# Performance work log

Hardware: AMD Instinct MI355X
Metric: run time of the kernel (lower is better)

Reference implementation:

```python
import jax, jax.numpy as jnp
import numpy as np

B, TE, TD, HE, HD = 16, 512, 64, 512, 512


def setup_inputs() -> dict:
    key = jax.random.key(0)
    k1, k2, k3, k4, k5 = jax.random.split(key, 5)
    return {
        "encoder_out_seq": jax.random.normal(k1, (B, TE, HE), dtype=jnp.float32),
        "decoder_out_seq": jax.random.normal(k2, (B, TD, HD), dtype=jnp.float32),
        "W_a": jax.random.normal(k3, (HE, HE), dtype=jnp.float32) * 0.05,
        "U_a": jax.random.normal(k4, (HD, HE), dtype=jnp.float32) * 0.05,
        "V_a": jax.random.normal(k5, (HE, 1), dtype=jnp.float32) * 0.05,
    }


def reference(encoder_out_seq, decoder_out_seq, W_a, U_a, V_a):
    # Bahdanau additive attention, batched over all decoder steps at once
    # (the original K.rnn loop over Td is embarrassingly parallel).
    Ws = jnp.einsum('bte,eh->bth', encoder_out_seq, W_a)   # [B,Te,He]
    Uh = jnp.einsum('bdk,kh->bdh', decoder_out_seq, U_a)   # [B,Td,He]
    # additive combine + tanh: [B,Td,Te,He]
    act = jnp.tanh(Ws[:, None, :, :] + Uh[:, :, None, :])
    e = jnp.einsum('bdth,h->bdt', act, V_a[:, 0])          # [B,Td,Te]
    e = jax.nn.softmax(e, axis=-1)                          # attention weights
    c = jnp.einsum('bdt,bth->bdh', e, encoder_out_seq)      # [B,Td,He] context
    return (c, e)
```

## Files before the change

kernel.cpp:

```cpp
#include <hip/hip_runtime.h>
#include <hip/hip_bf16.h>

#define BB 16
#define TE 512
#define TD 64
#define HE 512

#define PRESCALE 2.8853900817779268f

typedef __attribute__((ext_vector_type(8))) short bf16x8;
typedef __attribute__((ext_vector_type(4))) float f32x4;

__device__ __forceinline__ float fexp2(float x) {
#if __has_builtin(__builtin_amdgcn_exp2f)
    return __builtin_amdgcn_exp2f(x);
#else
    return exp2f(x);
#endif
}
__device__ __forceinline__ float frcp(float x) {
#if __has_builtin(__builtin_amdgcn_rcpf)
    return __builtin_amdgcn_rcpf(x);
#else
    return __fdividef(1.f, x);
#endif
}

__device__ __forceinline__ void split2(float x, unsigned short& h, unsigned short& l) {
    __hip_bfloat16 hb = __float2bfloat16(x);
    h = *(unsigned short*)&hb;
    float r = x - __bfloat162float(hb);
    __hip_bfloat16 lb = __float2bfloat16(r);
    l = *(unsigned short*)&lb;
}

__device__ __forceinline__ void gload16(const unsigned short* g, void* l) {
    __builtin_amdgcn_global_load_lds(
        (const __attribute__((address_space(1))) unsigned int*)g,
        (__attribute__((address_space(3))) unsigned int*)l, 16, 0, 0);
}



__device__ __forceinline__ void tile_load(const float* __restrict__ src, int ld,
                                          float (*tile)[64], int tid)
{
#pragma unroll
    for (int p = 0; p < 4; ++p) {
        const int f = p * 256 + tid;
        const int r = f >> 4, c4 = f & 15;
        const float4 v = *(const float4*)&src[(size_t)r * ld + c4 * 4];
        *(float4*)&tile[r][((c4 ^ (r & 7))) << 2] = v;
    }
}

__device__ __forceinline__ void tile_outA(float (*tile)[64],
                                          unsigned short* __restrict__ H,
                                          unsigned short* __restrict__ L,
                                          size_t Ms, size_t sg_base, size_t m_base, int tid)
{
#pragma unroll
    for (int p = 0; p < 2; ++p) {
        const int task = p * 256 + tid;
        const int s = task >> 6, mm = task & 63;
        const float4 x = *(const float4*)&tile[mm][(((s << 1)    ) ^ (mm & 7)) << 2];
        const float4 y = *(const float4*)&tile[mm][(((s << 1) | 1) ^ (mm & 7)) << 2];
        ushort4 ha, la, hb, lb;
        split2(x.x, ha.x, la.x); split2(x.y, ha.y, la.y);
        split2(x.z, ha.z, la.z); split2(x.w, ha.w, la.w);
        split2(y.x, hb.x, lb.x); split2(y.y, hb.y, lb.y);
        split2(y.z, hb.z, lb.z); split2(y.w, hb.w, lb.w);
        const size_t o = ((sg_base + s) * Ms + m_base + mm) * 8;
        *(ushort4*)&H[o] = ha; *(ushort4*)&H[o + 4] = hb;
        *(ushort4*)&L[o] = la; *(ushort4*)&L[o + 4] = lb;
    }
}

__device__ __forceinline__ void tile_outT(float (*tile)[64],
                                          unsigned short* __restrict__ H,
                                          unsigned short* __restrict__ L,
                                          size_t Ns, size_t sg_base, size_t n_base, int tid)
{
#pragma unroll
    for (int p = 0; p < 2; ++p) {
        const int task = p * 256 + tid;
        const int s2 = task >> 6, hh = task & 63;
        float v[8];
#pragma unroll
        for (int q = 0; q < 8; ++q) {
            const int r = s2 * 8 + q;
            v[q] = tile[r][((((hh >> 2)) ^ (r & 7)) << 2) + (hh & 3)];
        }
        ushort4 ha, la, hb, lb;
        split2(v[0], ha.x, la.x); split2(v[1], ha.y, la.y);
        split2(v[2], ha.z, la.z); split2(v[3], ha.w, la.w);
        split2(v[4], hb.x, lb.x); split2(v[5], hb.y, lb.y);
        split2(v[6], hb.z, lb.z); split2(v[7], hb.w, lb.w);
        const size_t o = ((sg_base + s2) * Ns + n_base + hh) * 8;
        *(ushort4*)&H[o] = ha; *(ushort4*)&H[o + 4] = hb;
        *(ushort4*)&L[o] = la; *(ushort4*)&L[o + 4] = lb;
    }
}

__global__ __launch_bounds__(256)
void split_enc_k8(const float* __restrict__ X,
                  unsigned short* __restrict__ Ah, unsigned short* __restrict__ Al,
                  unsigned short* __restrict__ Th, unsigned short* __restrict__ Tl)
{
    __shared__ float tile[64][64];
    const int tid = threadIdx.x;
    const int h0 = blockIdx.x * 64, t0 = blockIdx.y * 64, b = blockIdx.z;
    const size_t bo = (size_t)b * TE * HE;

    tile_load(X + bo + (size_t)t0 * HE + h0, HE, tile, tid);
    __syncthreads();

    tile_outA(tile, Ah, Al, (size_t)BB * TE, h0 >> 3, (size_t)b * TE + t0, tid);
    tile_outT(tile, Th + bo, Tl + bo, HE, t0 >> 3, h0, tid);
}

__global__ __launch_bounds__(256)
void split_misc_k8(const float* __restrict__ dec,
                   unsigned short* __restrict__ dH, unsigned short* __restrict__ dL,
                   const float* __restrict__ Wa,
                   unsigned short* __restrict__ wH, unsigned short* __restrict__ wL,
                   const float* __restrict__ Ua,
                   unsigned short* __restrict__ uH, unsigned short* __restrict__ uL)
{
    __shared__ float tile[64][64];
    const int tid = threadIdx.x;
    const int z = blockIdx.z;

    if (z == 2) {
        const int m0 = blockIdx.y * 64, h0 = blockIdx.x * 64;
        tile_load(dec + (size_t)m0 * HE + h0, HE, tile, tid);
        __syncthreads();
        tile_outA(tile, dH, dL, (size_t)BB * TD, h0 >> 3, m0, tid);
        return;
    }
    if (blockIdx.y >= 8) return;
    const float* X = z ? Ua : Wa;
    unsigned short* H = z ? uH : wH;
    unsigned short* L = z ? uL : wL;
    const int r0 = blockIdx.y * 64, c0 = blockIdx.x * 64;
    tile_load(X + (size_t)r0 * HE + c0, HE, tile, tid);
    __syncthreads();
    tile_outT(tile, H, L, HE, r0 >> 3, c0, tid);
}

__global__ __launch_bounds__(256)
void gemm_ws_uh(const unsigned short* __restrict__ eAh, const unsigned short* __restrict__ eAl,
                const unsigned short* __restrict__ wBh, const unsigned short* __restrict__ wBl,
                float* __restrict__ Ew,
                const unsigned short* __restrict__ dAh, const unsigned short* __restrict__ dAl,
                const unsigned short* __restrict__ uBh, const unsigned short* __restrict__ uBl,
                float* __restrict__ Eu)
{
    __shared__ char smem[2][32768];

    const int tid  = threadIdx.x;
    const int lane = tid & 63;
    const int wave = tid >> 6;
    const int wr = wave >> 1, wc = wave & 1;
    const int fr = lane & 15, fg = lane >> 4;

    const unsigned short *Ahi, *Alo, *Bhi, *Blo;
    float* C;
    int M, row0;
    if (blockIdx.y < 64) {
        Ahi = eAh; Alo = eAl; Bhi = wBh; Blo = wBl; C = Ew;
        M = BB * TE; row0 = blockIdx.y * 128;
    } else {
        Ahi = dAh; Alo = dAl; Bhi = uBh; Blo = uBl; C = Eu;
        M = BB * TD; row0 = (blockIdx.y - 64) * 128;
    }
    const int N = HE, K = HE;
    const int col0 = blockIdx.x * 128;

    f32x4 acc[4][4];
#pragma unroll
    for (int mi = 0; mi < 4; ++mi)
#pragma unroll
        for (int ni = 0; ni < 4; ++ni)
            acc[mi][ni] = (f32x4){0.f, 0.f, 0.f, 0.f};

    auto STAGE = [&](int buf, int k0) {
#pragma unroll
        for (int c = 0; c < 2; ++c) {
            const int bi  = (c * 4 + wave) * 64 + lane;
            const int g   = bi >> 7;
            const int idx = bi & 127;
            int mrow = row0 + idx; if (mrow >= M) mrow -= M;
            const int ncol = col0 + idx;
            const size_t ao = ((size_t)((k0 >> 3) + g) * M + mrow) * 8;
            const size_t bo = ((size_t)((k0 >> 3) + g) * N + ncol) * 8;
            const int lb = (c * 4 + wave) * 1024;
            gload16(Ahi + ao, smem[buf] + lb);
            gload16(Alo + ao, smem[buf] + 8192 + lb);
            gload16(Bhi + bo, smem[buf] + 16384 + lb);
            gload16(Blo + bo, smem[buf] + 24576 + lb);
        }
    };

    STAGE(0, 0);

    int buf = 0;
    for (int k0 = 0; k0 < K; k0 += 32) {
        if (k0 + 32 < K) {
            STAGE(buf ^ 1, k0 + 32);
            asm volatile("s_waitcnt vmcnt(8)\n\ts_barrier" ::: "memory");
        } else {
            asm volatile("s_waitcnt vmcnt(0)\n\ts_barrier" ::: "memory");
        }

        const int gb = fg << 7;
        bf16x8 ah[4], al[4], bh[4], bl[4];
#pragma unroll
        for (int mi = 0; mi < 4; ++mi) {
            const int off = (gb + wr * 64 + mi * 16 + fr) * 16;
            ah[mi] = *(const bf16x8*)(smem[buf] + off);
            al[mi] = *(const bf16x8*)(smem[buf] + 8192 + off);
        }
#pragma unroll
        for (int ni = 0; ni < 4; ++ni) {
            const int off = (gb + wc * 64 + ni * 16 + fr) * 16;
            bh[ni] = *(const bf16x8*)(smem[buf] + 16384 + off);
            bl[ni] = *(const bf16x8*)(smem[buf] + 24576 + off);
        }
#pragma unroll
        for (int mi = 0; mi < 4; ++mi)
#pragma unroll
            for (int ni = 0; ni < 4; ++ni) {
                acc[mi][ni] = __builtin_amdgcn_mfma_f32_16x16x32_bf16(ah[mi], bh[ni], acc[mi][ni], 0, 0, 0);
                acc[mi][ni] = __builtin_amdgcn_mfma_f32_16x16x32_bf16(ah[mi], bl[ni], acc[mi][ni], 0, 0, 0);
                acc[mi][ni] = __builtin_amdgcn_mfma_f32_16x16x32_bf16(al[mi], bh[ni], acc[mi][ni], 0, 0, 0);
            }
        asm volatile("s_barrier" ::: "memory");
        buf ^= 1;
    }

#pragma unroll
    for (int mi = 0; mi < 4; ++mi) {
        const int rbase = row0 + wr * 64 + mi * 16 + fg * 4;
#pragma unroll
        for (int ni = 0; ni < 4; ++ni) {
            const int col = col0 + wc * 64 + ni * 16 + fr;
#pragma unroll
            for (int r = 0; r < 4; ++r) {
                const int row = rbase + r;
                if (row < M) C[(size_t)row * N + col] = fexp2(acc[mi][ni][r] * PRESCALE);
            }
        }
    }
}

__global__ __launch_bounds__(256)
void gemm_mfma3(const unsigned short* __restrict__ Ahi, const unsigned short* __restrict__ Alo,
                const unsigned short* __restrict__ Bhi, const unsigned short* __restrict__ Blo,
                float* __restrict__ C, int M, int N, int K,
                long long sA, long long sB, long long sC)
{
    __shared__ char smem[2][32768];

    const int tid  = threadIdx.x;
    const int lane = tid & 63;
    const int wave = tid >> 6;
    const int wr = wave >> 1, wc = wave & 1;
    const int fr = lane & 15, fg = lane >> 4;
    const int row0 = blockIdx.y * 128;
    const int col0 = blockIdx.x * 128;

    Ahi += (size_t)blockIdx.z * sA; Alo += (size_t)blockIdx.z * sA;
    Bhi += (size_t)blockIdx.z * sB; Blo += (size_t)blockIdx.z * sB;
    C   += (size_t)blockIdx.z * sC;

    f32x4 acc[4][4];
#pragma unroll
    for (int mi = 0; mi < 4; ++mi)
#pragma unroll
        for (int ni = 0; ni < 4; ++ni)
            acc[mi][ni] = (f32x4){0.f, 0.f, 0.f, 0.f};

    auto STAGE = [&](int buf, int k0) {
#pragma unroll
        for (int c = 0; c < 2; ++c) {
            const int bi  = (c * 4 + wave) * 64 + lane;
            const int g   = bi >> 7;
            const int idx = bi & 127;
            int mrow = row0 + idx; if (mrow >= M) mrow -= M;
            const int ncol = col0 + idx;
            const size_t ao = ((size_t)((k0 >> 3) + g) * M + mrow) * 8;
            const size_t bo = ((size_t)((k0 >> 3) + g) * N + ncol) * 8;
            const int lb = (c * 4 + wave) * 1024;
            gload16(Ahi + ao, smem[buf] + lb);
            gload16(Alo + ao, smem[buf] + 8192 + lb);
            gload16(Bhi + bo, smem[buf] + 16384 + lb);
            gload16(Blo + bo, smem[buf] + 24576 + lb);
        }
    };

    STAGE(0, 0);

    int buf = 0;
    for (int k0 = 0; k0 < K; k0 += 32) {
        if (k0 + 32 < K) {
            STAGE(buf ^ 1, k0 + 32);
            asm volatile("s_waitcnt vmcnt(8)\n\ts_barrier" ::: "memory");
        } else {
            asm volatile("s_waitcnt vmcnt(0)\n\ts_barrier" ::: "memory");
        }

        const int gb = fg << 7;
        bf16x8 ah[4], al[4], bh[4], bl[4];
#pragma unroll
        for (int mi = 0; mi < 4; ++mi) {
            const int off = (gb + wr * 64 + mi * 16 + fr) * 16;
            ah[mi] = *(const bf16x8*)(smem[buf] + off);
            al[mi] = *(const bf16x8*)(smem[buf] + 8192 + off);
        }
#pragma unroll
        for (int ni = 0; ni < 4; ++ni) {
            const int off = (gb + wc * 64 + ni * 16 + fr) * 16;
            bh[ni] = *(const bf16x8*)(smem[buf] + 16384 + off);
            bl[ni] = *(const bf16x8*)(smem[buf] + 24576 + off);
        }
#pragma unroll
        for (int mi = 0; mi < 4; ++mi)
#pragma unroll
            for (int ni = 0; ni < 4; ++ni) {
                acc[mi][ni] = __builtin_amdgcn_mfma_f32_16x16x32_bf16(ah[mi], bh[ni], acc[mi][ni], 0, 0, 0);
                acc[mi][ni] = __builtin_amdgcn_mfma_f32_16x16x32_bf16(ah[mi], bl[ni], acc[mi][ni], 0, 0, 0);
                acc[mi][ni] = __builtin_amdgcn_mfma_f32_16x16x32_bf16(al[mi], bh[ni], acc[mi][ni], 0, 0, 0);
            }
        asm volatile("s_barrier" ::: "memory");
        buf ^= 1;
    }

#pragma unroll
    for (int mi = 0; mi < 4; ++mi) {
        const int rbase = row0 + wr * 64 + mi * 16 + fg * 4;
#pragma unroll
        for (int ni = 0; ni < 4; ++ni) {
            const int col = col0 + wc * 64 + ni * 16 + fr;
#pragma unroll
            for (int r = 0; r < 4; ++r) {
                const int row = rbase + r;
                if (row < M) C[(size_t)row * N + col] = acc[mi][ni][r];
            }
        }
    }
}

__global__ __launch_bounds__(256)
void gemm_f32(const float* __restrict__ A, const float* __restrict__ Bm,
              float* __restrict__ C, int M, int N, int K,
              long long sAb, long long sBb, long long sCb, float scale, int emode)
{
    __shared__ float As[16][68];
    __shared__ float Bs[16][68];

    const int tid = threadIdx.x;
    const int tx  = tid & 15;
    const int ty  = tid >> 4;
    const int row0 = blockIdx.y * 64;
    const int col0 = blockIdx.x * 64;

    A  += (long long)blockIdx.z * sAb;
    Bm += (long long)blockIdx.z * sBb;
    C  += (long long)blockIdx.z * sCb;

    float acc[4][4] = {};

    for (int k0 = 0; k0 < K; k0 += 16) {
        {
            const int r = tid >> 2;
            const int c = (tid & 3) * 4;
            const float4 av = *(const float4*)&A[(long long)(row0 + r) * K + k0 + c];
            As[c + 0][r] = av.x; As[c + 1][r] = av.y;
            As[c + 2][r] = av.z; As[c + 3][r] = av.w;
        }
        {
            const int r = tid >> 4;
            const int c = (tid & 15) * 4;
            *(float4*)&Bs[r][c] = *(const float4*)&Bm[(long long)(k0 + r) * N + col0 + c];
        }
        __syncthreads();

#pragma unroll
        for (int kk = 0; kk < 16; ++kk) {
            const float4 a = *(const float4*)&As[kk][ty * 4];
            const float4 b = *(const float4*)&Bs[kk][tx * 4];
            acc[0][0] += a.x * b.x; acc[0][1] += a.x * b.y; acc[0][2] += a.x * b.z; acc[0][3] += a.x * b.w;
            acc[1][0] += a.y * b.x; acc[1][1] += a.y * b.y; acc[1][2] += a.y * b.z; acc[1][3] += a.y * b.w;
            acc[2][0] += a.z * b.x; acc[2][1] += a.z * b.y; acc[2][2] += a.z * b.z; acc[2][3] += a.z * b.w;
            acc[3][0] += a.w * b.x; acc[3][1] += a.w * b.y; acc[3][2] += a.w * b.z; acc[3][3] += a.w * b.w;
        }
        __syncthreads();
    }

#pragma unroll
    for (int i = 0; i < 4; ++i) {
        float4 o;
        o.x = acc[i][0] * scale; o.y = acc[i][1] * scale;
        o.z = acc[i][2] * scale; o.w = acc[i][3] * scale;
        if (emode) { o.x = fexp2(o.x); o.y = fexp2(o.y); o.z = fexp2(o.z); o.w = fexp2(o.w); }
        *(float4*)&C[(long long)(row0 + ty * 4 + i) * N + col0 + tx * 4] = o;
    }
}

__global__ __launch_bounds__(256)
void scores_raw(const float* __restrict__ Ew, const float* __restrict__ Eu,
                const float* __restrict__ V, float* __restrict__ part)
{
    __shared__ float Ws_s[32][64];
    __shared__ float Uh_s[32][64];
    __shared__ float Vr_s[HE];

    const int tid = threadIdx.x;
    const int tg  = tid & 7;
    const int dg  = tid >> 3;

    const int tt0  = blockIdx.x * 32;
    const int quar = blockIdx.y & 3;
    const int d0   = (blockIdx.y >> 2) * 32;
    const int b    = blockIdx.z;

    const float* Wsg = Ew + (long long)b * TE * HE;
    const float* Uhg = Eu + ((long long)b * TD + d0) * HE;

    if (tid < 128) {
        const float4 v = *(const float4*)&V[tid * 4];
        float4 o; o.x = -2.f * v.x; o.y = -2.f * v.y; o.z = -2.f * v.z; o.w = -2.f * v.w;
        *(float4*)&Vr_s[tid * 4] = o;
    }

    float acc[4] = {0.f, 0.f, 0.f, 0.f};
    const int wswz = tg & 7;
    const int uswz = dg & 7;
    const int hbase = quar * (HE / 4);

    for (int hc = hbase; hc < hbase + HE / 4; hc += 64) {
        __syncthreads();
#pragma unroll
        for (int k = 0; k < 2; ++k) {
            const int idx = tid + k * 256;
            const int r   = idx >> 4;
            const int c4  = idx & 15;
            const float4 wv = *(const float4*)&Wsg[(long long)(tt0 + r) * HE + hc + c4 * 4];
            *(float4*)&Ws_s[r][(c4 ^ ((r >> 2) & 7)) * 4] = wv;
            const float4 uv = *(const float4*)&Uhg[(long long)r * HE + hc + c4 * 4];
            *(float4*)&Uh_s[r][(c4 ^ (r & 7)) * 4] = uv;
        }
        __syncthreads();

#pragma unroll 4
        for (int hs = 0; hs < 64; hs += 4) {
            const int h4 = hs >> 2;
            const float4 vv = *(const float4*)&Vr_s[hc + hs];
            const float4 u  = *(const float4*)&Uh_s[dg][(h4 ^ uswz) * 4];
#pragma unroll
            for (int i = 0; i < 4; ++i) {
                const float4 w = *(const float4*)&Ws_s[tg * 4 + i][(h4 ^ wswz) * 4];
                acc[i] = fmaf(vv.x, frcp(fmaf(w.x, u.x, 1.f)), acc[i]);
                acc[i] = fmaf(vv.y, frcp(fmaf(w.y, u.y, 1.f)), acc[i]);
                acc[i] = fmaf(vv.z, frcp(fmaf(w.z, u.z, 1.f)), acc[i]);
                acc[i] = fmaf(vv.w, frcp(fmaf(w.w, u.w, 1.f)), acc[i]);
            }
        }
    }

    float* dst = part + (size_t)quar * (BB * TD * TE);
    float4 o; o.x = acc[0]; o.y = acc[1]; o.z = acc[2]; o.w = acc[3];
    *(float4*)&dst[((long long)b * TD + d0 + dg) * TE + tt0 + tg * 4] = o;
}

__global__ __launch_bounds__(256)
void softmax_rows(const float* __restrict__ part, float* __restrict__ e,
                  unsigned short* __restrict__ H, unsigned short* __restrict__ L)
{
    const int lane = threadIdx.x & 63;
    const int wave = threadIdx.x >> 6;
    const long long row = blockIdx.x * 4 + wave;

    float4 a = {0.f, 0.f, 0.f, 0.f}, c = {0.f, 0.f, 0.f, 0.f};
#pragma unroll
    for (int q = 0; q < 4; ++q) {
        const float* p = part + (size_t)q * (BB * TD * TE) + row * TE;
        const float4 aq = *(const float4*)&p[lane * 4];
        const float4 cq = *(const float4*)&p[lane * 4 + 256];
        a.x += aq.x; a.y += aq.y; a.z += aq.z; a.w += aq.w;
        c.x += cq.x; c.y += cq.y; c.z += cq.z; c.w += cq.w;
    }

    float m = fmaxf(fmaxf(fmaxf(a.x, a.y), fmaxf(a.z, a.w)),
                    fmaxf(fmaxf(c.x, c.y), fmaxf(c.z, c.w)));
#pragma unroll
    for (int off = 32; off; off >>= 1) m = fmaxf(m, __shfl_xor(m, off));

    a.x = __expf(a.x - m); a.y = __expf(a.y - m); a.z = __expf(a.z - m); a.w = __expf(a.w - m);
    c.x = __expf(c.x - m); c.y = __expf(c.y - m); c.z = __expf(c.z - m); c.w = __expf(c.w - m);

    float s = (a.x + a.y + a.z + a.w) + (c.x + c.y + c.z + c.w);
#pragma unroll
    for (int off = 32; off; off >>= 1) s += __shfl_xor(s, off);

    const float inv = __fdividef(1.f, s);
    a.x *= inv; a.y *= inv; a.z *= inv; a.w *= inv;
    c.x *= inv; c.y *= inv; c.z *= inv; c.w *= inv;
    float* pe = e + row * TE;
    *(float4*)&pe[lane * 4] = a;
    *(float4*)&pe[lane * 4 + 256] = c;

    if (H) {
        const int b = (int)(row >> 6);
        const int d = (int)(row & 63);
        const size_t base = (size_t)b * (TD * TE);
        ushort4 h, l;
        {
            const int t0 = lane * 4;
            const size_t o = base + ((size_t)(t0 >> 3) * TD + d) * 8 + (t0 & 7);
            split2(a.x, h.x, l.x); split2(a.y, h.y, l.y);
            split2(a.z, h.z, l.z); split2(a.w, h.w, l.w);
            *(ushort4*)&H[o] = h;
            *(ushort4*)&L[o] = l;
        }
        {
            const int t0 = lane * 4 + 256;
            const size_t o = base + ((size_t)(t0 >> 3) * TD + d) * 8 + (t0 & 7);
            split2(c.x, h.x, l.x); split2(c.y, h.y, l.y);
            split2(c.z, h.z, l.z); split2(c.w, h.w, l.w);
            *(ushort4*)&H[o] = h;
            *(ushort4*)&L[o] = l;
        }
    }
}

extern "C" void kernel_launch(void* const* d_in, const int* in_sizes, int n_in,
                              void* d_out, int out_size, void* d_ws, size_t ws_size,
                              hipStream_t stream)
{
    const float* enc = (const float*)d_in[0];
    const float* dec = (const float*)d_in[1];
    const float* Wa  = (const float*)d_in[2];
    const float* Ua  = (const float*)d_in[3];
    const float* Va  = (const float*)d_in[4];

    float* out   = (float*)d_out;
    float* c_out = out;
    float* e_out = out + (size_t)BB * TD * HE;

    char* w = (char*)d_ws;
    float* Ew  = (float*)(w);
    float* Eu  = (float*)(w + 16777216);
    unsigned short* encAh = (unsigned short*)(w + 18874368);
    unsigned short* encAl = (unsigned short*)(w + 27262976);
    unsigned short* encTh = (unsigned short*)(w + 35651584);
    unsigned short* encTl = (unsigned short*)(w + 44040192);
    unsigned short* decAh = (unsigned short*)(w + 52428800);
    unsigned short* decAl = (unsigned short*)(w + 53477376);
    unsigned short* WaTh  = (unsigned short*)(w + 54525952);
    unsigned short* WaTl  = (unsigned short*)(w + 55050240);
    unsigned short* UaTh  = (unsigned short*)(w + 55574528);
    unsigned short* UaTl  = (unsigned short*)(w + 56098816);
    unsigned short* eh    = (unsigned short*)(w + 56623104);
    unsigned short* el    = (unsigned short*)(w + 57671680);
    float* part = (float*)(w + 58720256);
    const size_t REQUIRED = 67108864;

    dim3 blk(256);

    if (ws_size >= REQUIRED) {
        split_enc_k8<<<dim3(HE / 64, TE / 64, BB), blk, 0, stream>>>(
            enc, encAh, encAl, encTh, encTl);
        split_misc_k8<<<dim3(8, 16, 3), blk, 0, stream>>>(
            dec, decAh, decAl, Wa, WaTh, WaTl, Ua, UaTh, UaTl);

        gemm_ws_uh<<<dim3(4, 72, 1), blk, 0, stream>>>(
            encAh, encAl, WaTh, WaTl, Ew, decAh, decAl, UaTh, UaTl, Eu);

        scores_raw<<<dim3(TE / 32, (TD / 32) * 4, BB), blk, 0, stream>>>(Ew, Eu, Va, part);
        softmax_rows<<<dim3(BB * TD / 4), blk, 0, stream>>>(part, e_out, eh, el);

        gemm_mfma3<<<dim3(4, 1, BB), blk, 0, stream>>>(
            eh, el, encTh, encTl, c_out, TD, HE, TE,
            (long long)TD * TE, (long long)TE * HE, (long long)TD * HE);
    } else {
        float* pf = (float*)(w + 18874368);
        gemm_f32<<<dim3(HE / 64, (BB * TE) / 64, 1), blk, 0, stream>>>(
            enc, Wa, Ew, BB * TE, HE, HE, 0, 0, 0, PRESCALE, 1);
        gemm_f32<<<dim3(HE / 64, (BB * TD) / 64, 1), blk, 0, stream>>>(
            dec, Ua, Eu, BB * TD, HE, HE, 0, 0, 0, PRESCALE, 1);
        scores_raw<<<dim3(TE / 32, (TD / 32) * 4, BB), blk, 0, stream>>>(Ew, Eu, Va, pf);
        softmax_rows<<<dim3(BB * TD / 4), blk, 0, stream>>>(pf, e_out, nullptr, nullptr);
        gemm_f32<<<dim3(HE / 64, TD / 64, BB), blk, 0, stream>>>(
            e_out, enc, c_out, TD, HE, TE,
            (long long)TD * TE, (long long)TE * HE, (long long)TD * HE, 1.0f, 0);
    }
}
```

Baseline: 90.70 us.

## Merge split kernels and remap block indices for XCD-aware L2 locality

Fuses the encoder split and misc split kernels into one launch, removing a kernel launch and the gap between the two. It also remaps the linear block index in the projection GEMM and the scores kernel with a stride-8 permutation, so consecutive blocks that share operands land on the same XCD and its L2. The split_all grid has idle blocks (y 9..15 for z<16), which cost a little launch overhead.

Result: faster. 87.36 us (-3.7%).

```diff
diff --git a/kernel.cpp b/kernel.cpp
--- a/kernel.cpp
+++ b/kernel.cpp
@@ -39,7 +39,6 @@
         (const __attribute__((address_space(1))) unsigned int*)g,
         (__attribute__((address_space(3))) unsigned int*)l, 16, 0, 0);
 }
-
 
 
 __device__ __forceinline__ void tile_load(const float* __restrict__ src, int ld,
@@ -103,46 +102,41 @@
 }
 
 __global__ __launch_bounds__(256)
-void split_enc_k8(const float* __restrict__ X,
-                  unsigned short* __restrict__ Ah, unsigned short* __restrict__ Al,
-                  unsigned short* __restrict__ Th, unsigned short* __restrict__ Tl)
+void split_all(const float* __restrict__ enc,
+               unsigned short* __restrict__ eAh, unsigned short* __restrict__ eAl,
+               unsigned short* __restrict__ eTh, unsigned short* __restrict__ eTl,
+               const float* __restrict__ dec,
+               unsigned short* __restrict__ dH, unsigned short* __restrict__ dL,
+               const float* __restrict__ Wa,
+               unsigned short* __restrict__ wH, unsigned short* __restrict__ wL,
+               const float* __restrict__ Ua,
+               unsigned short* __restrict__ uH, unsigned short* __restrict__ uL)
 {
     __shared__ float tile[64][64];
     const int tid = threadIdx.x;
-    const int h0 = blockIdx.x * 64, t0 = blockIdx.y * 64, b = blockIdx.z;
-    const size_t bo = (size_t)b * TE * HE;
-
-    tile_load(X + bo + (size_t)t0 * HE + h0, HE, tile, tid);
-    __syncthreads();
-
-    tile_outA(tile, Ah, Al, (size_t)BB * TE, h0 >> 3, (size_t)b * TE + t0, tid);
-    tile_outT(tile, Th + bo, Tl + bo, HE, t0 >> 3, h0, tid);
-}
-
-__global__ __launch_bounds__(256)
-void split_misc_k8(const float* __restrict__ dec,
-                   unsigned short* __restrict__ dH, unsigned short* __restrict__ dL,
-                   const float* __restrict__ Wa,
-                   unsigned short* __restrict__ wH, unsigned short* __restrict__ wL,
-                   const float* __restrict__ Ua,
-                   unsigned short* __restrict__ uH, unsigned short* __restrict__ uL)
-{
-    __shared__ float tile[64][64];
-    const int tid = threadIdx.x;
-    const int z = blockIdx.z;
-
-    if (z == 2) {
-        const int m0 = blockIdx.y * 64, h0 = blockIdx.x * 64;
-        tile_load(dec + (size_t)m0 * HE + h0, HE, tile, tid);
-        __syncthreads();
-        tile_outA(tile, dH, dL, (size_t)BB * TD, h0 >> 3, m0, tid);
+    const int x = blockIdx.x, y = blockIdx.y, z = blockIdx.z;
+
+    if (z < 16) {
+        if (y < 8) {
+            const int h0 = x * 64, t0 = y * 64;
+            const size_t bo = (size_t)z * TE * HE;
+            tile_load(enc + bo + (size_t)t0 * HE + h0, HE, tile, tid);
+            __syncthreads();
+            tile_outA(tile, eAh, eAl, (size_t)BB * TE, h0 >> 3, (size_t)z * TE + t0, tid);
+            tile_outT(tile, eTh + bo, eTl + bo, HE, t0 >> 3, h0, tid);
+        } else if (y == 8) {
+            const int m0 = z * 64, h0 = x * 64;
+            tile_load(dec + (size_t)m0 * HE + h0, HE, tile, tid);
+            __syncthreads();
+            tile_outA(tile, dH, dL, (size_t)BB * TD, h0 >> 3, m0, tid);
+        }
         return;
     }
-    if (blockIdx.y >= 8) return;
-    const float* X = z ? Ua : Wa;
-    unsigned short* H = z ? uH : wH;
-    unsigned short* L = z ? uL : wL;
-    const int r0 = blockIdx.y * 64, c0 = blockIdx.x * 64;
+    const int yy = (y < 8) ? y : y - 8;
+    const float* X = (y < 8) ? Wa : Ua;
+    unsigned short* H = (y < 8) ? wH : uH;
+    unsigned short* L = (y < 8) ? wL : uL;
+    const int r0 = yy * 64, c0 = x * 64;
     tile_load(X + (size_t)r0 * HE + c0, HE, tile, tid);
     __syncthreads();
     tile_outT(tile, H, L, HE, r0 >> 3, c0, tid);
@@ -164,18 +158,22 @@
     const int wr = wave >> 1, wc = wave & 1;
     const int fr = lane & 15, fg = lane >> 4;
 
+    const int hw = blockIdx.y * 4 + blockIdx.x;
+    const int f  = (hw & 7) * 36 + (hw >> 3);
+    const int bx = f & 3, by = f >> 2;
+
     const unsigned short *Ahi, *Alo, *Bhi, *Blo;
     float* C;
     int M, row0;
-    if (blockIdx.y < 64) {
+    if (by < 64) {
         Ahi = eAh; Alo = eAl; Bhi = wBh; Blo = wBl; C = Ew;
-        M = BB * TE; row0 = blockIdx.y * 128;
+        M = BB * TE; row0 = by * 128;
     } else {
         Ahi = dAh; Alo = dAl; Bhi = uBh; Blo = uBl; C = Eu;
-        M = BB * TD; row0 = (blockIdx.y - 64) * 128;
+        M = BB * TD; row0 = (by - 64) * 128;
     }
     const int N = HE, K = HE;
-    const int col0 = blockIdx.x * 128;
+    const int col0 = bx * 128;
 
     f32x4 acc[4][4];
 #pragma unroll
@@ -358,34 +356,24 @@
 {
     __shared__ float As[16][68];
     __shared__ float Bs[16][68];
-
     const int tid = threadIdx.x;
-    const int tx  = tid & 15;
-    const int ty  = tid >> 4;
-    const int row0 = blockIdx.y * 64;
-    const int col0 = blockIdx.x * 64;
-
-    A  += (long long)blockIdx.z * sAb;
-    Bm += (long long)blockIdx.z * sBb;
-    C  += (long long)blockIdx.z * sCb;
-
+    const int tx = tid & 15, ty = tid >> 4;
+    const int row0 = blockIdx.y * 64, col0 = blockIdx.x * 64;
+    A += (long long)blockIdx.z * sAb; Bm += (long long)blockIdx.z * sBb;
+    C += (long long)blockIdx.z * sCb;
     float acc[4][4] = {};
-
     for (int k0 = 0; k0 < K; k0 += 16) {
         {
-            const int r = tid >> 2;
-            const int c = (tid & 3) * 4;
+            const int r = tid >> 2, c = (tid & 3) * 4;
             const float4 av = *(const float4*)&A[(long long)(row0 + r) * K + k0 + c];
             As[c + 0][r] = av.x; As[c + 1][r] = av.y;
             As[c + 2][r] = av.z; As[c + 3][r] = av.w;
         }
         {
-            const int r = tid >> 4;
-            const int c = (tid & 15) * 4;
+            const int r = tid >> 4, c = (tid & 15) * 4;
             *(float4*)&Bs[r][c] = *(const float4*)&Bm[(long long)(k0 + r) * N + col0 + c];
         }
         __syncthreads();
-
 #pragma unroll
         for (int kk = 0; kk < 16; ++kk) {
             const float4 a = *(const float4*)&As[kk][ty * 4];
@@ -397,7 +385,6 @@
         }
         __syncthreads();
     }
-
 #pragma unroll
     for (int i = 0; i < 4; ++i) {
         float4 o;
@@ -420,10 +407,14 @@
     const int tg  = tid & 7;
     const int dg  = tid >> 3;
 
-    const int tt0  = blockIdx.x * 32;
-    const int quar = blockIdx.y & 3;
-    const int d0   = (blockIdx.y >> 2) * 32;
-    const int b    = blockIdx.z;
+    const int hw = (blockIdx.z * 8 + blockIdx.y) * 16 + blockIdx.x;
+    const int w_ = (hw & 7) * 256 + (hw >> 3);
+    const int yy = w_ & 7;
+    const int zx = w_ >> 3;
+    const int tt0  = (zx & 15) * 32;
+    const int quar = yy & 3;
+    const int d0   = (yy >> 2) * 32;
+    const int b    = zx >> 4;
 
     const float* Wsg = Ew + (long long)b * TE * HE;
     const float* Uhg = Eu + ((long long)b * TD + d0) * HE;
@@ -570,9 +561,8 @@
     dim3 blk(256);
 
     if (ws_size >= REQUIRED) {
-        split_enc_k8<<<dim3(HE / 64, TE / 64, BB), blk, 0, stream>>>(
-            enc, encAh, encAl, encTh, encTl);
-        split_misc_k8<<<dim3(8, 16, 3), blk, 0, stream>>>(
+        split_all<<<dim3(8, 16, 17), blk, 0, stream>>>(
+            enc, encAh, encAl, encTh, encTl,
             dec, decAh, decAl, Wa, WaTh, WaTl, Ua, UaTh, UaTl);
 
         gemm_ws_uh<<<dim3(4, 72, 1), blk, 0, stream>>>(
```
